# Optimization experiments

Hardware: AMD Instinct MI355X
Metric: run time of the kernel (lower is better)

## Reference

```python
import jax, jax.numpy as jnp
import numpy as np

# ---- configuration (matches init_kwargs / input_specs) ----
N = 48        # velocity grid points per axis (unum = vnum = wnum)
B = 8         # spatial cells (batch)
QUAD = 8      # radial Gauss-Legendre quadrature points
OMEGA = 0.81  # VHS exponent used in the radial kernel weight r**omega
M_ANG = 5     # sphere-quadrature resolution -> M*(M-1) angle pairs
VMAX = 5.0    # velocity domain [-VMAX, VMAX]^3


def _besselj1(x):
    # Numerical Recipes rational approximation of J1(x), numpy, setup-time only.
    x = np.asarray(x, dtype=np.float64)
    ax = np.abs(x)
    y = x * x
    p1 = x * (72362614232.0 + y * (-7895059235.0 + y * (242396853.1
         + y * (-2972611.439 + y * (15704.48260 + y * (-30.16036606))))))
    q1 = 144725228442.0 + y * (2300535178.0 + y * (18583304.74
         + y * (99447.43394 + y * (376.9991397 + y))))
    small = p1 / q1
    axs = np.where(ax > 0, ax, 1.0)
    z = 8.0 / axs
    y2 = z * z
    p2 = 1.0 + y2 * (0.183105e-2 + y2 * (-0.3516396496e-4
         + y2 * (0.2457520174e-5 + y2 * (-0.240337019e-6))))
    q2 = 0.04687499995 + y2 * (-0.2002690873e-3 + y2 * (0.8449199096e-5
         + y2 * (-0.88228987e-6 + y2 * 0.105787412e-6)))
    xx = axs - 2.356194491  # ax - 3*pi/4
    big = np.sqrt(0.636619772 / axs) * (np.cos(xx) * p2 - z * np.sin(xx) * q2) * np.sign(x)
    return np.where(ax < 8.0, small, big)


def _init_kernel_mode_vector(n, quad_num, omega, m, vmax):
    # Fast spectral method precompute (Mouhot-Pareschi), mirrors init_kernel_mode_vector.
    pi = np.pi
    du = 2.0 * vmax / (n - 1)
    fre = np.arange(-(n // 2), n // 2).astype(np.float64) * (2.0 * pi / (n * du))
    supp = np.sqrt(2.0) * 2.0 * vmax / (3.0 + np.sqrt(2.0))
    xg, wg = np.polynomial.legendre.leggauss(quad_num)  # on [-1,1]
    r = 0.5 * supp * (xg + 1.0)   # radial abscissa on [0, supp]
    gw = 0.5 * supp * wg          # radial weights
    ta = pi / m * np.arange(1, m)      # (m-1,) polar angles
    tb = pi / m * np.arange(1, m + 1)  # (m,)  azimuthal angles
    st = np.sin(ta)[:, None, None, None, None]
    ct = np.cos(ta)[:, None, None, None, None]
    cb = np.cos(tb)[None, :, None, None, None]
    sb = np.sin(tb)[None, :, None, None, None]
    fx = fre[:, None, None]
    fy = fre[None, :, None]
    fz = fre[None, None, :]
    # s[a,b,i,j,k] = <freq, sigma(theta_a, theta2_b)>
    s = st * cb * fx + st * sb * fy + (ct * np.ones_like(sb)) * fz
    phi = np.zeros_like(s)
    for q in range(quad_num):  # small fixed quadrature loop (setup only)
        phi += 2.0 * gw[q] * (r[q] ** omega) * np.cos(s * r[q])
    phi *= st
    s2 = (fx ** 2 + fy ** 2 + fz ** 2) - s ** 2
    pos = s2 > 1e-12
    sr = np.sqrt(np.where(pos, s2, 1.0))
    psi = np.where(pos, 2.0 * pi * supp * _besselj1(supp * sr) / sr, pi * supp ** 2)
    phipsi = (phi * psi).sum(axis=(0, 1))
    t = (m - 1) * m
    return (phi.reshape(t, n, n, n).astype(np.float32),
            psi.reshape(t, n, n, n).astype(np.float32),
            phipsi.astype(np.float32))


def setup_inputs() -> dict:
    key = jax.random.key(0)
    k1, _ = jax.random.split(key)
    phi, psi, phipsi = _init_kernel_mode_vector(N, QUAD, OMEGA, M_ANG, VMAX)
    f = jax.random.uniform(k1, (B, N * N * N), dtype=jnp.float32)
    return {
        "f": f,
        "kn_bzm": jnp.ones((), dtype=jnp.float32),
        "phi": jnp.asarray(phi),
        "psi": jnp.asarray(psi),
        "phipsi": jnp.asarray(phipsi),
        "M": M_ANG,
    }


def reference(f, kn_bzm, phi, psi, phipsi, M):
    # do_collision: reshape flat velocity dim to 3D grid, run collision_fft.
    n = phi.shape[-1]
    axes = (-3, -2, -1)
    f3 = f.reshape(f.shape[:-1] + (n, n, n))
    nvel = n * n * n
    # normalized, shifted spectrum of f
    f_spec = jnp.fft.fftshift(
        jnp.fft.fftn(f3.astype(jnp.complex64), axes=axes) / nvel, axes=axes)
    # gain term: sum over M*(M-1) angle pairs of fft(f_spec*phi_t) * fft(f_spec*psi_t)
    fs = f_spec[..., None, :, :, :]                       # [B, 1, n, n, n]
    fg = (jnp.fft.fftn(fs * phi, axes=axes) *
          jnp.fft.fftn(fs * psi, axes=axes)).sum(axis=-4)  # [B, n, n, n]
    # loss term
    fl = (jnp.fft.fftn(f_spec * phipsi, axes=axes) *
          jnp.fft.fftn(f_spec, axes=axes))
    scale = (4.0 * jnp.pi ** 2) / kn_bzm / (M * M)
    Q = scale * (fg - fl).real
    return Q.reshape(f.shape).astype(f.dtype)
```

## Files before the change

### kernel.cpp

```cpp
#include <hip/hip_runtime.h>
#include <math.h>

#define NN 48
#define NP 49
#define N2 2304
#define N3 110592
#define NB 8
#define NT 20
#define NH 25
#define NSL 7

typedef float2 cplx;

#define CMAC(AR, AI, D, Wv)                                        \
    AR = fmaf((D).x, (Wv).x, AR); AR = fmaf(-(D).y, (Wv).y, AR);   \
    AI = fmaf((D).x, (Wv).y, AI); AI = fmaf((D).y, (Wv).x, AI);

__device__ __forceinline__ void twinit(cplx* W, int t) {
    if (t < NN) {
        float ang = -6.28318530717958647692f * (float)t / (float)NN;
        float s, c;
        sincosf(ang, &s, &c);
        W[t] = make_float2(c, s);
    }
}

__device__ __forceinline__ void radix3_combine(
    float s0r, float s0i, float s1r, float s1i, float s2r, float s2i,
    cplx w1, cplx w2, cplx& X0, cplx& X1, cplx& X2)
{
    float y1r = s1r*w1.x - s1i*w1.y, y1i = s1r*w1.y + s1i*w1.x;
    float y2r = s2r*w2.x - s2i*w2.y, y2i = s2r*w2.y + s2i*w2.x;
    float ar = y1r + y2r, ai = y1i + y2i;
    float br = y1r - y2r, bi = y1i - y2i;
    X0 = make_float2(s0r + ar, s0i + ai);
    float mr = s0r - 0.5f*ar, mi = s0i - 0.5f*ai;
    const float h = 0.86602540378443864676f;
    X1 = make_float2(mr + h*bi, mi - h*br);
    X2 = make_float2(mr - h*bi, mi + h*br);
}

__device__ __forceinline__ void dft_rows(cplx (*S)[NP], const cplx* W, int t, int shift) {
    const int rg = t >> 4;
    const int j  = t & 15;
    float ar[3][3], ai[3][3];
#pragma unroll
    for (int q = 0; q < 3; ++q)
#pragma unroll
        for (int r = 0; r < 3; ++r) { ar[q][r] = 0.f; ai[q][r] = 0.f; }
    const int step = 3 * j;
    int tw = 0;
#pragma unroll 4
    for (int n1 = 0; n1 < 16; ++n1) {
        cplx w = W[tw];
#pragma unroll
        for (int q = 0; q < 3; ++q) {
            const cplx* row = S[3*rg + q];
            cplx d0 = row[3*n1+0], d1 = row[3*n1+1], d2 = row[3*n1+2];
            CMAC(ar[q][0], ai[q][0], d0, w);
            CMAC(ar[q][1], ai[q][1], d1, w);
            CMAC(ar[q][2], ai[q][2], d2, w);
        }
        tw += step; if (tw >= NN) tw -= NN;
    }
    cplx w1 = W[j], w2 = W[2*j];
    __syncthreads();
    int k0 = j, k1 = j + 16, k2 = j + 32;
    if (shift) { k0 = (k0+24)%NN; k1 = (k1+24)%NN; k2 = (k2+24)%NN; }
#pragma unroll
    for (int q = 0; q < 3; ++q) {
        cplx X0, X1, X2;
        radix3_combine(ar[q][0],ai[q][0],ar[q][1],ai[q][1],ar[q][2],ai[q][2],w1,w2,X0,X1,X2);
        S[3*rg+q][k0] = X0; S[3*rg+q][k1] = X1; S[3*rg+q][k2] = X2;
    }
    __syncthreads();
}

__device__ __forceinline__ void dft_cols(cplx (*S)[NP], const cplx* W, int t, int shift) {
    const int zg = t & 15;
    const int j  = t >> 4;
    float ar[3][3], ai[3][3];
#pragma unroll
    for (int zi = 0; zi < 3; ++zi)
#pragma unroll
        for (int r = 0; r < 3; ++r) { ar[zi][r] = 0.f; ai[zi][r] = 0.f; }
    const int step = 3 * j;
    int tw = 0;
#pragma unroll 4
    for (int n1 = 0; n1 < 16; ++n1) {
        cplx w = W[tw];
#pragma unroll
        for (int r = 0; r < 3; ++r) {
            const cplx* row = S[3*n1 + r];
            cplx d0 = row[3*zg+0], d1 = row[3*zg+1], d2 = row[3*zg+2];
            CMAC(ar[0][r], ai[0][r], d0, w);
            CMAC(ar[1][r], ai[1][r], d1, w);
            CMAC(ar[2][r], ai[2][r], d2, w);
        }
        tw += step; if (tw >= NN) tw -= NN;
    }
    cplx w1 = W[j], w2 = W[2*j];
    __syncthreads();
    int k0 = j, k1 = j + 16, k2 = j + 32;
    if (shift) { k0 = (k0+24)%NN; k1 = (k1+24)%NN; k2 = (k2+24)%NN; }
#pragma unroll
    for (int zi = 0; zi < 3; ++zi) {
        cplx X0, X1, X2;
        radix3_combine(ar[zi][0],ai[zi][0],ar[zi][1],ai[zi][1],ar[zi][2],ai[zi][2],w1,w2,X0,X1,X2);
        S[k0][3*zg+zi] = X0; S[k1][3*zg+zi] = X1; S[k2][3*zg+zi] = X2;
    }
    __syncthreads();
}

__global__ __launch_bounds__(256)
void kA_f(const float* __restrict__ f, cplx* __restrict__ out) {
    __shared__ cplx S[NN][NP];
    __shared__ cplx W[NN];
    const int x = blockIdx.x, b = blockIdx.y, t = threadIdx.x;
    const float* src = f + (size_t)b * N3 + (size_t)x * N2;
    for (int i = t; i < N2; i += 256) S[i / NN][i % NN] = make_float2(src[i], 0.f);
    twinit(W, t);
    __syncthreads();
    dft_rows(S, W, t, 1);
    dft_cols(S, W, t, 1);
    cplx* dst = out + (size_t)b * N3 + (size_t)x * N2;
    for (int i = t; i < N2; i += 256) dst[i] = S[i / NN][i % NN];
}

__global__ __launch_bounds__(256)
void kB_f(cplx* __restrict__ vol) {
    __shared__ cplx S[NN][NP];
    __shared__ cplx W[NN];
    const int y = blockIdx.x, b = blockIdx.y, t = threadIdx.x;
    cplx* base = vol + (size_t)b * N3 + (size_t)y * NN;
    for (int i = t; i < N2; i += 256) { int xr = i / NN, z = i % NN; S[xr][z] = base[(size_t)xr * N2 + z]; }
    twinit(W, t);
    __syncthreads();
    dft_cols(S, W, t, 1);
    const float inv = 1.f / (float)N3;
    for (int i = t; i < N2; i += 256) {
        int xr = i / NN, z = i % NN;
        cplx v = S[xr][z];
        base[(size_t)xr * N2 + z] = make_float2(v.x * inv, v.y * inv);
    }
}

__global__ __launch_bounds__(256)
void kA_mul(const cplx* __restrict__ spec,
            const float* __restrict__ phi, const float* __restrict__ psi,
            const float* __restrict__ phipsi,
            cplx* __restrict__ va, cplx* __restrict__ vb, int t0) {
    __shared__ cplx S[NN][NP];
    __shared__ cplx W[NN];
    const int ix = blockIdx.x, b = blockIdx.y, t = threadIdx.x;
    const int lt = blockIdx.z >> 1, term = blockIdx.z & 1;
    const int ti = t0 + lt;
    const float* mul;
    if (ti < NT) mul = (term ? psi : phi) + (size_t)ti * N3 + (size_t)ix * N2;
    else         mul = term ? (const float*)nullptr : (phipsi + (size_t)ix * N2);
    const cplx* src = spec + (size_t)b * N3 + (size_t)ix * N2;
    cplx* out = (term ? vb : va) + ((size_t)(lt * NB + b) * NH + ix) * N2;
    for (int i = t; i < N2; i += 256) {
        cplx v = src[i];
        if (mul) { float m = mul[i]; v.x *= m; v.y *= m; }
        S[i / NN][i % NN] = v;
    }
    twinit(W, t);
    __syncthreads();
    dft_rows(S, W, t, 0);
    dft_cols(S, W, t, 0);
    for (int i = t; i < N2; i += 256) out[i] = S[i / NN][i % NN];
}

__global__ __launch_bounds__(256)
void kB_all(const cplx* __restrict__ va, const cplx* __restrict__ vb,
            float* __restrict__ out, const float* __restrict__ kn,
            const int* __restrict__ Mv, int t0, int cn) {
    __shared__ cplx SA[NH][NP];
    __shared__ cplx SB[NH][NP];
    __shared__ cplx W[NN];
    const int y = blockIdx.x, b = blockIdx.y, s = blockIdx.z, t = threadIdx.x;
    twinit(W, t);
    const int zg = t & 15, jg = t >> 4;
    float qr[3][3];
#pragma unroll
    for (int m = 0; m < 3; ++m)
#pragma unroll
        for (int zi = 0; zi < 3; ++zi) qr[m][zi] = 0.f;

    for (int lt = s; lt < cn; lt += NSL) {
        const int ti = t0 + lt;
        const cplx* pa = va + (size_t)(lt * NB + b) * NH * N2 + (size_t)y * NN;
        const cplx* pb = vb + (size_t)(lt * NB + b) * NH * N2 + (size_t)y * NN;
        for (int i = t; i < NH * NN; i += 256) {
            int n = i / NN, z = i % NN;
            SA[n][z] = pa[(size_t)n * N2 + z];
            SB[n][z] = pb[(size_t)n * N2 + z];
        }
        __syncthreads();
        float sa[3][3], sb[3][3];
#pragma unroll
        for (int m = 0; m < 3; ++m)
#pragma unroll
            for (int zi = 0; zi < 3; ++zi) { sa[m][zi] = 0.f; sb[m][zi] = 0.f; }
        int m0 = jg, m1 = jg + 16, m2 = jg + 32;
        const int s0 = jg, s1 = jg + 16, s2 = jg + 32;
        for (int n = 1; n <= 23; ++n) {
            cplx w0 = W[m0], w1 = W[m1], w2 = W[m2];
#pragma unroll
            for (int zi = 0; zi < 3; ++zi) {
                cplx A = SA[n][3*zg+zi];
                cplx B = SB[n][3*zg+zi];
                sa[0][zi] = fmaf(A.x, w0.x, sa[0][zi]); sa[0][zi] = fmaf(-A.y, w0.y, sa[0][zi]);
                sa[1][zi] = fmaf(A.x, w1.x, sa[1][zi]); sa[1][zi] = fmaf(-A.y, w1.y, sa[1][zi]);
                sa[2][zi] = fmaf(A.x, w2.x, sa[2][zi]); sa[2][zi] = fmaf(-A.y, w2.y, sa[2][zi]);
                sb[0][zi] = fmaf(B.x, w0.x, sb[0][zi]); sb[0][zi] = fmaf(-B.y, w0.y, sb[0][zi]);
                sb[1][zi] = fmaf(B.x, w1.x, sb[1][zi]); sb[1][zi] = fmaf(-B.y, w1.y, sb[1][zi]);
                sb[2][zi] = fmaf(B.x, w2.x, sb[2][zi]); sb[2][zi] = fmaf(-B.y, w2.y, sb[2][zi]);
            }
            m0 += s0; if (m0 >= NN) m0 -= NN;
            m1 += s1; if (m1 >= NN) m1 -= NN;
            m2 += s2; if (m2 >= NN) m2 -= NN;
        }
        const float sgn = (jg & 1) ? -1.f : 1.f;
        const float wgt = (ti == NT) ? -1.f : 1.f;
#pragma unroll
        for (int zi = 0; zi < 3; ++zi) {
            float e0a  = SA[0][3*zg+zi].x,  e24a = SA[24][3*zg+zi].x;
            float e0b  = SB[0][3*zg+zi].x,  e24b = SB[24][3*zg+zi].x;
            float basea = e0a + sgn * e24a;
            float baseb = e0b + sgn * e24b;
#pragma unroll
            for (int m = 0; m < 3; ++m) {
                float Ah = basea + 2.f * sa[m][zi];
                float Bh = baseb + 2.f * sb[m][zi];
                qr[m][zi] += wgt * Ah * Bh;
            }
        }
        __syncthreads();
    }
    float mf = (float)(Mv[0] * Mv[0]);
    float scale = 4.f * 3.14159265358979323846f * 3.14159265358979323846f / (kn[0] * mf);
#pragma unroll
    for (int m = 0; m < 3; ++m) {
        int j = jg + 16 * m;
#pragma unroll
        for (int zi = 0; zi < 3; ++zi) {
            int z = 3 * zg + zi;
            size_t idx = (size_t)b * N3 + (size_t)j * N2 + (size_t)y * NN + z;
            atomicAdd(&out[idx], scale * qr[m][zi]);
        }
    }
}

extern "C" void kernel_launch(void* const* d_in, const int* in_sizes, int n_in,
                              void* d_out, int out_size, void* d_ws, size_t ws_size,
                              hipStream_t stream) {
    const float* f      = (const float*)d_in[0];
    const float* kn     = (const float*)d_in[1];
    const float* phi    = (const float*)d_in[2];
    const float* psi    = (const float*)d_in[3];
    const float* phipsi = (const float*)d_in[4];
    const int*   Mv     = (const int*)d_in[5];
    float* out = (float*)d_out;

    char* w = (char*)d_ws;
    const size_t fspecB = (size_t)NB * N3 * sizeof(cplx);
    const size_t perTB  = (size_t)NB * NH * N2 * sizeof(cplx);
    cplx* fspec = (cplx*)w;
    char* pool  = w + fspecB;

    const int NTOT = NT + 1;
    size_t avail = (ws_size > fspecB) ? (ws_size - fspecB) : 0;
    int chunk = (int)(avail / (2 * perTB));
    if (chunk < 1)    chunk = 1;
    if (chunk > NTOT) chunk = NTOT;
    cplx* va = (cplx*)pool;
    cplx* vb = (cplx*)(pool + (size_t)chunk * perTB);

    hipMemsetAsync(out, 0, (size_t)NB * N3 * sizeof(float), stream);

    kA_f<<<dim3(NN, NB), 256, 0, stream>>>(f, fspec);
    kB_f<<<dim3(NN, NB), 256, 0, stream>>>(fspec);

    for (int t0 = 0; t0 < NTOT; t0 += chunk) {
        int cn = (t0 + chunk <= NTOT) ? chunk : (NTOT - t0);
        kA_mul<<<dim3(NH, NB, 2 * cn), 256, 0, stream>>>(
            fspec, phi, psi, phipsi, va, vb, t0);
        kB_all<<<dim3(NN, NB, NSL), 256, 0, stream>>>(va, vb, out, kn, Mv, t0, cn);
    }
}
```

Measured before the change: 306.1 us.

## Pack phi and psi transforms into float4 to share twiddles and source loads

New measurement: 290.2 us. 1.05x faster.

```diff
diff --git a/kernel.cpp b/kernel.cpp
--- a/kernel.cpp
+++ b/kernel.cpp
@@ -15,6 +15,12 @@
 #define CMAC(AR, AI, D, Wv)                                        \
     AR = fmaf((D).x, (Wv).x, AR); AR = fmaf(-(D).y, (Wv).y, AR);   \
     AI = fmaf((D).x, (Wv).y, AI); AI = fmaf((D).y, (Wv).x, AI);
+
+#define CMAC4(AC, D, Wv)                                             \
+    (AC).x = fmaf((D).x, (Wv).x, (AC).x); (AC).x = fmaf(-(D).y, (Wv).y, (AC).x); \
+    (AC).y = fmaf((D).x, (Wv).y, (AC).y); (AC).y = fmaf((D).y, (Wv).x, (AC).y); \
+    (AC).z = fmaf((D).z, (Wv).x, (AC).z); (AC).z = fmaf(-(D).w, (Wv).y, (AC).z); \
+    (AC).w = fmaf((D).z, (Wv).y, (AC).w); (AC).w = fmaf((D).w, (Wv).x, (AC).w);
 
 __device__ __forceinline__ void twinit(cplx* W, int t) {
     if (t < NN) {
@@ -40,6 +46,18 @@
     X2 = make_float2(mr - h*bi, mi + h*br);
 }
 
+__device__ __forceinline__ void radix3_combine4(
+    float4 s0, float4 s1, float4 s2, cplx w1, cplx w2,
+    float4& X0, float4& X1, float4& X2)
+{
+    cplx a0, a1, a2, b0, b1, b2;
+    radix3_combine(s0.x, s0.y, s1.x, s1.y, s2.x, s2.y, w1, w2, a0, a1, a2);
+    radix3_combine(s0.z, s0.w, s1.z, s1.w, s2.z, s2.w, w1, w2, b0, b1, b2);
+    X0 = make_float4(a0.x, a0.y, b0.x, b0.y);
+    X1 = make_float4(a1.x, a1.y, b1.x, b1.y);
+    X2 = make_float4(a2.x, a2.y, b2.x, b2.y);
+}
+
 __device__ __forceinline__ void dft_rows(cplx (*S)[NP], const cplx* W, int t, int shift) {
     const int rg = t >> 4;
     const int j  = t & 15;
@@ -108,6 +126,75 @@
         cplx X0, X1, X2;
         radix3_combine(ar[zi][0],ai[zi][0],ar[zi][1],ai[zi][1],ar[zi][2],ai[zi][2],w1,w2,X0,X1,X2);
         S[k0][3*zg+zi] = X0; S[k1][3*zg+zi] = X1; S[k2][3*zg+zi] = X2;
+    }
+    __syncthreads();
+}
+
+__device__ __forceinline__ void dft_rows4(float4 (*S)[NP], const cplx* W, int t) {
+    const int rg = t >> 4;
+    const int j  = t & 15;
+    float4 acc[3][3];
+#pragma unroll
+    for (int q = 0; q < 3; ++q)
+#pragma unroll
+        for (int r = 0; r < 3; ++r) acc[q][r] = make_float4(0.f,0.f,0.f,0.f);
+    const int step = 3 * j;
+    int tw = 0;
+    const float4* r0 = S[3*rg + 0];
+    const float4* r1 = S[3*rg + 1];
+    const float4* r2 = S[3*rg + 2];
+#pragma unroll 4
+    for (int n1 = 0; n1 < 16; ++n1) {
+        cplx w = W[tw];
+        float4 d00 = r0[3*n1+0], d01 = r0[3*n1+1], d02 = r0[3*n1+2];
+        float4 d10 = r1[3*n1+0], d11 = r1[3*n1+1], d12 = r1[3*n1+2];
+        float4 d20 = r2[3*n1+0], d21 = r2[3*n1+1], d22 = r2[3*n1+2];
+        CMAC4(acc[0][0], d00, w); CMAC4(acc[0][1], d01, w); CMAC4(acc[0][2], d02, w);
+        CMAC4(acc[1][0], d10, w); CMAC4(acc[1][1], d11, w); CMAC4(acc[1][2], d12, w);
+        CMAC4(acc[2][0], d20, w); CMAC4(acc[2][1], d21, w); CMAC4(acc[2][2], d22, w);
+        tw += step; if (tw >= NN) tw -= NN;
+    }
+    cplx w1 = W[j], w2 = W[2*j];
+    __syncthreads();
+#pragma unroll
+    for (int q = 0; q < 3; ++q) {
+        float4 X0, X1, X2;
+        radix3_combine4(acc[q][0], acc[q][1], acc[q][2], w1, w2, X0, X1, X2);
+        S[3*rg+q][j] = X0; S[3*rg+q][j+16] = X1; S[3*rg+q][j+32] = X2;
+    }
+    __syncthreads();
+}
+
+__device__ __forceinline__ void dft_cols4(float4 (*S)[NP], const cplx* W, int t) {
+    const int zg = t & 15;
+    const int j  = t >> 4;
+    float4 acc[3][3];
+#pragma unroll
+    for (int zi = 0; zi < 3; ++zi)
+#pragma unroll
+        for (int r = 0; r < 3; ++r) acc[zi][r] = make_float4(0.f,0.f,0.f,0.f);
+    const int step = 3 * j;
+    int tw = 0;
+#pragma unroll 4
+    for (int n1 = 0; n1 < 16; ++n1) {
+        cplx w = W[tw];
+#pragma unroll
+        for (int r = 0; r < 3; ++r) {
+            const float4* row = S[3*n1 + r];
+            float4 d0 = row[3*zg+0], d1 = row[3*zg+1], d2 = row[3*zg+2];
+            CMAC4(acc[0][r], d0, w);
+            CMAC4(acc[1][r], d1, w);
+            CMAC4(acc[2][r], d2, w);
+        }
+        tw += step; if (tw >= NN) tw -= NN;
+    }
+    cplx w1 = W[j], w2 = W[2*j];
+    __syncthreads();
+#pragma unroll
+    for (int zi = 0; zi < 3; ++zi) {
+        float4 X0, X1, X2;
+        radix3_combine4(acc[zi][0], acc[zi][1], acc[zi][2], w1, w2, X0, X1, X2);
+        S[j][3*zg+zi] = X0; S[j+16][3*zg+zi] = X1; S[j+32][3*zg+zi] = X2;
     }
     __syncthreads();
 }
@@ -146,38 +233,38 @@
 }
 
 __global__ __launch_bounds__(256)
-void kA_mul(const cplx* __restrict__ spec,
-            const float* __restrict__ phi, const float* __restrict__ psi,
-            const float* __restrict__ phipsi,
-            cplx* __restrict__ va, cplx* __restrict__ vb, int t0) {
-    __shared__ cplx S[NN][NP];
+void kAB(const cplx* __restrict__ spec,
+         const float* __restrict__ phi, const float* __restrict__ psi,
+         const float* __restrict__ phipsi,
+         float4* __restrict__ vab, int t0) {
+    __shared__ float4 S[NN][NP];
     __shared__ cplx W[NN];
-    const int ix = blockIdx.x, b = blockIdx.y, t = threadIdx.x;
-    const int lt = blockIdx.z >> 1, term = blockIdx.z & 1;
+    const int ix = blockIdx.x, b = blockIdx.y, lt = blockIdx.z, t = threadIdx.x;
     const int ti = t0 + lt;
-    const float* mul;
-    if (ti < NT) mul = (term ? psi : phi) + (size_t)ti * N3 + (size_t)ix * N2;
-    else         mul = term ? (const float*)nullptr : (phipsi + (size_t)ix * N2);
     const cplx* src = spec + (size_t)b * N3 + (size_t)ix * N2;
-    cplx* out = (term ? vb : va) + ((size_t)(lt * NB + b) * NH + ix) * N2;
+    const float* mp;
+    const float* mq;
+    if (ti < NT) { mp = phi + (size_t)ti * N3 + (size_t)ix * N2; mq = psi + (size_t)ti * N3 + (size_t)ix * N2; }
+    else         { mp = phipsi + (size_t)ix * N2;               mq = (const float*)nullptr; }
     for (int i = t; i < N2; i += 256) {
         cplx v = src[i];
-        if (mul) { float m = mul[i]; v.x *= m; v.y *= m; }
-        S[i / NN][i % NN] = v;
+        float p = mp[i];
+        float q = mq ? mq[i] : 1.f;
+        S[i / NN][i % NN] = make_float4(v.x * p, v.y * p, v.x * q, v.y * q);
     }
     twinit(W, t);
     __syncthreads();
-    dft_rows(S, W, t, 0);
-    dft_cols(S, W, t, 0);
+    dft_rows4(S, W, t);
+    dft_cols4(S, W, t);
+    float4* out = vab + ((size_t)(lt * NB + b) * NH + ix) * N2;
     for (int i = t; i < N2; i += 256) out[i] = S[i / NN][i % NN];
 }
 
 __global__ __launch_bounds__(256)
-void kB_all(const cplx* __restrict__ va, const cplx* __restrict__ vb,
+void kB_all(const float4* __restrict__ vab,
             float* __restrict__ out, const float* __restrict__ kn,
             const int* __restrict__ Mv, int t0, int cn) {
-    __shared__ cplx SA[NH][NP];
-    __shared__ cplx SB[NH][NP];
+    __shared__ float4 SAB[NH][NP];
     __shared__ cplx W[NN];
     const int y = blockIdx.x, b = blockIdx.y, s = blockIdx.z, t = threadIdx.x;
     twinit(W, t);
@@ -190,12 +277,10 @@
 
     for (int lt = s; lt < cn; lt += NSL) {
         const int ti = t0 + lt;
-        const cplx* pa = va + (size_t)(lt * NB + b) * NH * N2 + (size_t)y * NN;
-        const cplx* pb = vb + (size_t)(lt * NB + b) * NH * N2 + (size_t)y * NN;
+        const float4* pa = vab + (size_t)(lt * NB + b) * NH * N2 + (size_t)y * NN;
         for (int i = t; i < NH * NN; i += 256) {
             int n = i / NN, z = i % NN;
-            SA[n][z] = pa[(size_t)n * N2 + z];
-            SB[n][z] = pb[(size_t)n * N2 + z];
+            SAB[n][z] = pa[(size_t)n * N2 + z];
         }
         __syncthreads();
         float sa[3][3], sb[3][3];
@@ -209,14 +294,13 @@
             cplx w0 = W[m0], w1 = W[m1], w2 = W[m2];
 #pragma unroll
             for (int zi = 0; zi < 3; ++zi) {
-                cplx A = SA[n][3*zg+zi];
-                cplx B = SB[n][3*zg+zi];
-                sa[0][zi] = fmaf(A.x, w0.x, sa[0][zi]); sa[0][zi] = fmaf(-A.y, w0.y, sa[0][zi]);
-                sa[1][zi] = fmaf(A.x, w1.x, sa[1][zi]); sa[1][zi] = fmaf(-A.y, w1.y, sa[1][zi]);
-                sa[2][zi] = fmaf(A.x, w2.x, sa[2][zi]); sa[2][zi] = fmaf(-A.y, w2.y, sa[2][zi]);
-                sb[0][zi] = fmaf(B.x, w0.x, sb[0][zi]); sb[0][zi] = fmaf(-B.y, w0.y, sb[0][zi]);
-                sb[1][zi] = fmaf(B.x, w1.x, sb[1][zi]); sb[1][zi] = fmaf(-B.y, w1.y, sb[1][zi]);
-                sb[2][zi] = fmaf(B.x, w2.x, sb[2][zi]); sb[2][zi] = fmaf(-B.y, w2.y, sb[2][zi]);
+                float4 d = SAB[n][3*zg+zi];
+                sa[0][zi] = fmaf(d.x, w0.x, sa[0][zi]); sa[0][zi] = fmaf(-d.y, w0.y, sa[0][zi]);
+                sa[1][zi] = fmaf(d.x, w1.x, sa[1][zi]); sa[1][zi] = fmaf(-d.y, w1.y, sa[1][zi]);
+                sa[2][zi] = fmaf(d.x, w2.x, sa[2][zi]); sa[2][zi] = fmaf(-d.y, w2.y, sa[2][zi]);
+                sb[0][zi] = fmaf(d.z, w0.x, sb[0][zi]); sb[0][zi] = fmaf(-d.w, w0.y, sb[0][zi]);
+                sb[1][zi] = fmaf(d.z, w1.x, sb[1][zi]); sb[1][zi] = fmaf(-d.w, w1.y, sb[1][zi]);
+                sb[2][zi] = fmaf(d.z, w2.x, sb[2][zi]); sb[2][zi] = fmaf(-d.w, w2.y, sb[2][zi]);
             }
             m0 += s0; if (m0 >= NN) m0 -= NN;
             m1 += s1; if (m1 >= NN) m1 -= NN;
@@ -226,10 +310,10 @@
         const float wgt = (ti == NT) ? -1.f : 1.f;
 #pragma unroll
         for (int zi = 0; zi < 3; ++zi) {
-            float e0a  = SA[0][3*zg+zi].x,  e24a = SA[24][3*zg+zi].x;
-            float e0b  = SB[0][3*zg+zi].x,  e24b = SB[24][3*zg+zi].x;
-            float basea = e0a + sgn * e24a;
-            float baseb = e0b + sgn * e24b;
+            float4 e0  = SAB[0][3*zg+zi];
+            float4 e24 = SAB[24][3*zg+zi];
+            float basea = e0.x + sgn * e24.x;
+            float baseb = e0.z + sgn * e24.z;
 #pragma unroll
             for (int m = 0; m < 3; ++m) {
                 float Ah = basea + 2.f * sa[m][zi];
@@ -266,17 +350,16 @@
 
     char* w = (char*)d_ws;
     const size_t fspecB = (size_t)NB * N3 * sizeof(cplx);
-    const size_t perTB  = (size_t)NB * NH * N2 * sizeof(cplx);
+    const size_t perTB  = (size_t)NB * NH * N2 * sizeof(float4);
     cplx* fspec = (cplx*)w;
     char* pool  = w + fspecB;
 
     const int NTOT = NT + 1;
     size_t avail = (ws_size > fspecB) ? (ws_size - fspecB) : 0;
-    int chunk = (int)(avail / (2 * perTB));
+    int chunk = (int)(avail / perTB);
     if (chunk < 1)    chunk = 1;
     if (chunk > NTOT) chunk = NTOT;
-    cplx* va = (cplx*)pool;
-    cplx* vb = (cplx*)(pool + (size_t)chunk * perTB);
+    float4* vab = (float4*)pool;
 
     hipMemsetAsync(out, 0, (size_t)NB * N3 * sizeof(float), stream);
 
@@ -285,8 +368,7 @@
 
     for (int t0 = 0; t0 < NTOT; t0 += chunk) {
         int cn = (t0 + chunk <= NTOT) ? chunk : (NTOT - t0);
-        kA_mul<<<dim3(NH, NB, 2 * cn), 256, 0, stream>>>(
-            fspec, phi, psi, phipsi, va, vb, t0);
-        kB_all<<<dim3(NN, NB, NSL), 256, 0, stream>>>(va, vb, out, kn, Mv, t0, cn);
-    }
-}
+        kAB<<<dim3(NH, NB, cn), 256, 0, stream>>>(fspec, phi, psi, phipsi, vab, t0);
+        kB_all<<<dim3(NN, NB, NSL), 256, 0, stream>>>(vab, out, kn, Mv, t0, cn);
+    }
+}
```
